# Performance work log

Measured on AMD Instinct MI355X. Metric: run time of the kernel, lower is better.

Reference implementation:

```python
import jax, jax.numpy as jnp
import numpy as np

N_NODES = 100000
N_EDGES = 3200000
VM, VA, PG, QG, PD, QD = 0, 1, 2, 3, 4, 5
G, B = 0, 1


def setup_inputs() -> dict:
    key = jax.random.key(0)
    k1, k2, k3, k4, k5 = jax.random.split(key, 5)
    pred = jax.random.normal(k1, (N_NODES, 6), dtype=jnp.float32)
    target = jax.random.normal(k2, (N_NODES, 6), dtype=jnp.float32)
    edge_index = jax.random.randint(k3, (2, N_EDGES), 0, N_NODES, dtype=jnp.int64)
    edge_attr = jax.random.normal(k4, (N_EDGES, 2), dtype=jnp.float32)
    mask = jax.random.randint(k5, (N_NODES, 6), 0, 2) == 1
    return {"pred": pred, "target": target, "edge_index": edge_index,
            "edge_attr": edge_attr, "mask": mask}


def reference(pred, target, edge_index, edge_attr, mask):
    # temp_pred[~mask] = target[~mask]
    temp_pred = jnp.where(mask, pred, target)
    vm = temp_pred[:, VM]
    va = temp_pred[:, VA]
    pg = temp_pred[:, PG]
    qg = temp_pred[:, QG]
    pd = temp_pred[:, PD]
    qd = temp_pred[:, QD]
    g = edge_attr[:, G]
    b = edge_attr[:, B]
    src, dst = edge_index[0], edge_index[1]

    v_from = vm[src]                      # [E] gather
    v_to = vm[dst]
    ang = va[src] - va[dst]
    c, s = jnp.cos(ang), jnp.sin(ang)
    vv = v_from * v_to
    p_flow = vv * (g * c + b * s)         # [E]
    q_flow = vv * (g * s - b * c)

    # scatter-add flows into source nodes
    p_calc = jax.ops.segment_sum(p_flow, src, num_segments=N_NODES)
    q_calc = jax.ops.segment_sum(q_flow, src, num_segments=N_NODES)

    p_imb = pg - pd - p_calc
    q_imb = qg - qd - q_calc
    loss = jnp.mean(p_imb ** 2) + jnp.mean(q_imb ** 2)
    return loss
```

## Files before the change

kernel.cpp:

```cpp
#include <hip/hip_runtime.h>
#include <cstdint>

#define N_NODES 100000
#define N_EDGES 3200000
#define SPAN    256
#define SHIFT   8
#define NB      ((N_NODES + SPAN - 1) / SPAN)
#define CHUNK   4096
#define BTH     512
#define NITER   (CHUNK / BTH)
#define NBLK    ((N_EDGES + CHUNK - 1) / CHUNK)
#define PREF_W  (NB + 1)

__global__ __launch_bounds__(256)
void prep_kernel(const float* __restrict__ pred,
                 const float* __restrict__ target,
                 const void* __restrict__ mask,
                 float2* __restrict__ u_tab,
                 float2* __restrict__ base_pq,
                 float* __restrict__ d_out, int out_size) {
    __shared__ int s_mask8;
    if (threadIdx.x < 64) {
        uint32_t w = ((const uint32_t*)mask)[threadIdx.x];
        bool nz = (w & 0xFFFFFF00u) != 0u;
        unsigned long long m = __ballot(nz);
        if (threadIdx.x == 0) s_mask8 = (m != 0ull) ? 1 : 0;
    }
    if (blockIdx.x == 0 && threadIdx.x == 0)
        for (int k = 0; k < out_size; ++k) d_out[k] = 0.0f;
    __syncthreads();

    int i = blockIdx.x * 256 + threadIdx.x;
    if (i >= N_NODES) return;

    const float2* p2 = (const float2*)pred;
    const float2* t2 = (const float2*)target;
    float2 pa = p2[3 * i], pb = p2[3 * i + 1], pc = p2[3 * i + 2];
    float2 ta = t2[3 * i], tb = t2[3 * i + 1], tc = t2[3 * i + 2];
    float pr[6] = {pa.x, pa.y, pb.x, pb.y, pc.x, pc.y};
    float tg[6] = {ta.x, ta.y, tb.x, tb.y, tc.x, tc.y};
    int mk[6];
    if (s_mask8) {
        const uint16_t* mu = (const uint16_t*)mask;
        uint16_t m0 = mu[3 * i], m1 = mu[3 * i + 1], m2 = mu[3 * i + 2];
        mk[0] = m0 & 0xFF; mk[1] = m0 >> 8;
        mk[2] = m1 & 0xFF; mk[3] = m1 >> 8;
        mk[4] = m2 & 0xFF; mk[5] = m2 >> 8;
    } else {
        const int2* mi = (const int2*)mask;
        int2 m0 = mi[3 * i], m1 = mi[3 * i + 1], m2 = mi[3 * i + 2];
        mk[0] = m0.x; mk[1] = m0.y; mk[2] = m1.x;
        mk[3] = m1.y; mk[4] = m2.x; mk[5] = m2.y;
    }
    float tp[6];
    #pragma unroll
    for (int j = 0; j < 6; ++j) tp[j] = mk[j] ? pr[j] : tg[j];

    float s, c;
    sincosf(tp[1], &s, &c);
    u_tab[i]   = make_float2(tp[0] * c, tp[0] * s);
    base_pq[i] = make_float2(tp[2] - tp[4], tp[3] - tp[5]);
}

__global__ __launch_bounds__(BTH)
void bin_kernel(const void* __restrict__ edge_index,
                const float2* __restrict__ edge_attr,
                const float2* __restrict__ u_tab,
                uint2* __restrict__ recs,
                uint16_t* __restrict__ pref_T) {
    __shared__ uint2 s_rec[CHUNK];
    __shared__ uint32_t s_cnt[NB];
    __shared__ uint32_t s_pref[PREF_W];
    __shared__ uint32_t s_wsum[8], s_woff[8];
    __shared__ int s_i64;

    const int tid = threadIdx.x;
    const int lane = tid & 63, wid = tid >> 6;
    if (tid < 64) {
        uint32_t w = ((const uint32_t*)edge_index)[tid];
        bool nz = (tid & 1) && (w != 0u);
        unsigned long long m = __ballot(nz);
        if (tid == 0) s_i64 = (m == 0ull) ? 1 : 0;
    }
    if (tid < NB) s_cnt[tid] = 0u;
    __syncthreads();
    const bool is64 = (s_i64 != 0);
    const int ebase = blockIdx.x * CHUNK;
    const int nE = min(CHUNK, N_EDGES - ebase);

    uint32_t src_r[NITER];
    #pragma unroll
    for (int it = 0; it < NITER; ++it) {
        int j = it * BTH + tid;
        uint32_t s = 0u;
        if (j < nE) {
            int e = ebase + j;
            s = is64 ? (uint32_t)((const unsigned long long*)edge_index)[e]
                     : ((const uint32_t*)edge_index)[e];
            atomicAdd(&s_cnt[s >> SHIFT], 1u);
        }
        src_r[it] = s;
    }
    __syncthreads();

    {
        uint32_t v0 = (tid < NB) ? s_cnt[tid] : 0u;
        uint32_t x = v0;
        #pragma unroll
        for (int off = 1; off < 64; off <<= 1) {
            uint32_t y = (uint32_t)__shfl_up((int)x, off, 64);
            if (lane >= off) x += y;
        }
        if (lane == 63) s_wsum[wid] = x;
        __syncthreads();
        if (tid < 8) {
            uint32_t w0 = s_wsum[tid];
            uint32_t xx = w0;
            #pragma unroll
            for (int off = 1; off < 8; off <<= 1) {
                uint32_t y = (uint32_t)__shfl_up((int)xx, off, 64);
                if (tid >= off) xx += y;
            }
            s_woff[tid] = xx - w0;
        }
        __syncthreads();
        uint32_t incl = x + s_woff[wid];
        if (tid < NB) s_pref[tid + 1] = incl;
        if (tid == 0) s_pref[0] = 0u;
        if (tid < NB) s_cnt[tid] = 0u;
        __syncthreads();
    }

    #pragma unroll
    for (int it = 0; it < NITER; ++it) {
        int j = it * BTH + tid;
        if (j < nE) {
            int e = ebase + j;
            uint32_t dst = is64
                ? (uint32_t)((const unsigned long long*)edge_index)[(size_t)N_EDGES + e]
                : ((const uint32_t*)edge_index)[(size_t)N_EDGES + e];
            float2 gb = edge_attr[e];
            float2 u  = u_tab[dst];
            float vr = gb.x * u.x - gb.y * u.y;
            float vi = -(gb.y * u.x + gb.x * u.y);
            uint32_t nid = src_r[it];
            uint32_t bk = nid >> SHIFT, lid = nid & (SPAN - 1);
            uint32_t r = atomicAdd(&s_cnt[bk], 1u);
            uint2 rc;
            rc.x = (__float_as_uint(vr) & ~0xFFu) | lid;
            rc.y = __float_as_uint(vi);
            s_rec[s_pref[bk] + r] = rc;
        }
    }
    __syncthreads();

    {
        const uint4* s4 = (const uint4*)s_rec;
        uint4* a4 = (uint4*)(recs + (size_t)blockIdx.x * CHUNK);
        for (int k = tid; k < nE / 2; k += BTH) a4[k] = s4[k];
        if ((nE & 1) && tid == 0)
            recs[(size_t)blockIdx.x * CHUNK + nE - 1] = s_rec[nE - 1];
    }
    for (int b = tid; b < PREF_W; b += BTH)
        pref_T[(size_t)b * NBLK + blockIdx.x] = (uint16_t)s_pref[b];
}

__global__ __launch_bounds__(1024)
void reduce_kernel(const uint2* __restrict__ recs,
                   const uint16_t* __restrict__ pref_T,
                   const float2* __restrict__ u_tab,
                   const float2* __restrict__ base_pq,
                   float* __restrict__ d_out) {
    __shared__ float2 s_acc[4][SPAN];
    __shared__ float s_part[16];
    if (threadIdx.x < SPAN) {
        #pragma unroll
        for (int r = 0; r < 4; ++r) s_acc[r][threadIdx.x] = make_float2(0.0f, 0.0f);
    }
    __syncthreads();

    const int b = blockIdx.x;
    const int rep = (threadIdx.x >> 6) & 3;
    if (threadIdx.x < NBLK) {
        uint32_t s = pref_T[(size_t)b * NBLK + threadIdx.x];
        uint32_t e = pref_T[(size_t)(b + 1) * NBLK + threadIdx.x];
        const uint2* arena = recs + (size_t)threadIdx.x * CHUNK;
        uint32_t j = s;
        for (; j + 2 <= e; j += 2) {
            uint2 r0 = arena[j];
            uint2 r1 = arena[j + 1];
            atomicAdd(&s_acc[rep][r0.x & 0xFFu].x, __uint_as_float(r0.x & ~0xFFu));
            atomicAdd(&s_acc[rep][r0.x & 0xFFu].y, __uint_as_float(r0.y));
            atomicAdd(&s_acc[rep][r1.x & 0xFFu].x, __uint_as_float(r1.x & ~0xFFu));
            atomicAdd(&s_acc[rep][r1.x & 0xFFu].y, __uint_as_float(r1.y));
        }
        if (j < e) {
            uint2 rc = arena[j];
            atomicAdd(&s_acc[rep][rc.x & 0xFFu].x, __uint_as_float(rc.x & ~0xFFu));
            atomicAdd(&s_acc[rep][rc.x & 0xFFu].y, __uint_as_float(rc.y));
        }
    }
    __syncthreads();

    float v = 0.0f;
    int node = b * SPAN + (int)threadIdx.x;
    if (threadIdx.x < SPAN && node < N_NODES) {
        float2 S = make_float2(0.0f, 0.0f);
        #pragma unroll
        for (int rr = 0; rr < 4; ++rr) {
            float2 t = s_acc[rr][threadIdx.x];
            S.x += t.x; S.y += t.y;
        }
        float2 ui = u_tab[node];
        float2 bp = base_pq[node];
        float pc = ui.x * S.x - ui.y * S.y;
        float qc = ui.x * S.y + ui.y * S.x;
        float p = bp.x - pc, q = bp.y - qc;
        v = p * p + q * q;
    }
    #pragma unroll
    for (int off = 32; off > 0; off >>= 1) v += __shfl_down(v, off, 64);
    if ((threadIdx.x & 63) == 0) s_part[threadIdx.x >> 6] = v;
    __syncthreads();
    if (threadIdx.x == 0) {
        float t = 0.0f;
        #pragma unroll
        for (int w = 0; w < 16; ++w) t += s_part[w];
        atomicAdd(d_out, t * (1.0f / (float)N_NODES));
    }
}

extern "C" void kernel_launch(void* const* d_in, const int* in_sizes, int n_in,
                              void* d_out, int out_size, void* d_ws, size_t ws_size,
                              hipStream_t stream) {
    const float*  pred       = (const float*)d_in[0];
    const float*  target     = (const float*)d_in[1];
    const void*   edge_index = d_in[2];
    const float2* edge_attr  = (const float2*)d_in[3];
    const void*   mask       = d_in[4];
    float* out = (float*)d_out;

    char* ws = (char*)d_ws;
    float2*   u_tab   = (float2*)ws;
    float2*   base_pq = (float2*)(ws + 800000);
    uint16_t* pref_T  = (uint16_t*)(ws + 1600000);
    uint2*    recs    = (uint2*)(ws + 2400000);

    prep_kernel<<<(N_NODES + 255) / 256, 256, 0, stream>>>(
        pred, target, mask, u_tab, base_pq, out, out_size);

    bin_kernel<<<NBLK, BTH, 0, stream>>>(
        edge_index, edge_attr, u_tab, recs, pref_T);

    reduce_kernel<<<NB, 1024, 0, stream>>>(
        recs, pref_T, u_tab, base_pq, out);
}
```

Measured before the change: 173.9 us.

## Double bin chunk size and split each reduce segment across two threads

The binning chunk grows to 8192 edges with 1024-thread blocks. This halves the number of producer blocks and the size of the transposed prefix table, and lets the record arena move closer in the workspace. In the reduce kernel, each producer segment is split between two threads, so 782 threads stay busy despite fewer producers. Each thread reads records pairwise with 16-byte loads after aligning to an even index. The risks are lower bin-kernel block count (391 blocks), heavier LDS use per block, and dropping the odd-tail store, which relies on every chunk length being even.

```diff
diff --git a/kernel.cpp b/kernel.cpp
--- a/kernel.cpp
+++ b/kernel.cpp
@@ -6,8 +6,8 @@
 #define SPAN    256
 #define SHIFT   8
 #define NB      ((N_NODES + SPAN - 1) / SPAN)
-#define CHUNK   4096
-#define BTH     512
+#define CHUNK   8192
+#define BTH     1024
 #define NITER   (CHUNK / BTH)
 #define NBLK    ((N_EDGES + CHUNK - 1) / CHUNK)
 #define PREF_W  (NB + 1)
@@ -71,7 +71,7 @@
     __shared__ uint2 s_rec[CHUNK];
     __shared__ uint32_t s_cnt[NB];
     __shared__ uint32_t s_pref[PREF_W];
-    __shared__ uint32_t s_wsum[8], s_woff[8];
+    __shared__ uint32_t s_wsum[16], s_woff[16];
     __shared__ int s_i64;
 
     const int tid = threadIdx.x;
@@ -113,11 +113,11 @@
         }
         if (lane == 63) s_wsum[wid] = x;
         __syncthreads();
-        if (tid < 8) {
+        if (tid < 16) {
             uint32_t w0 = s_wsum[tid];
             uint32_t xx = w0;
             #pragma unroll
-            for (int off = 1; off < 8; off <<= 1) {
+            for (int off = 1; off < 16; off <<= 1) {
                 uint32_t y = (uint32_t)__shfl_up((int)xx, off, 64);
                 if (tid >= off) xx += y;
             }
@@ -158,8 +158,6 @@
         const uint4* s4 = (const uint4*)s_rec;
         uint4* a4 = (uint4*)(recs + (size_t)blockIdx.x * CHUNK);
         for (int k = tid; k < nE / 2; k += BTH) a4[k] = s4[k];
-        if ((nE & 1) && tid == 0)
-            recs[(size_t)blockIdx.x * CHUNK + nE - 1] = s_rec[nE - 1];
     }
     for (int b = tid; b < PREF_W; b += BTH)
         pref_T[(size_t)b * NBLK + blockIdx.x] = (uint16_t)s_pref[b];
@@ -181,18 +179,26 @@
 
     const int b = blockIdx.x;
     const int rep = (threadIdx.x >> 6) & 3;
-    if (threadIdx.x < NBLK) {
-        uint32_t s = pref_T[(size_t)b * NBLK + threadIdx.x];
-        uint32_t e = pref_T[(size_t)(b + 1) * NBLK + threadIdx.x];
-        const uint2* arena = recs + (size_t)threadIdx.x * CHUNK;
-        uint32_t j = s;
+    if (threadIdx.x < 2 * NBLK) {
+        const int prod = (threadIdx.x < NBLK) ? threadIdx.x : threadIdx.x - NBLK;
+        const int half = (threadIdx.x < NBLK) ? 0 : 1;
+        uint32_t s0 = pref_T[(size_t)b * NBLK + prod];
+        uint32_t e0 = pref_T[(size_t)(b + 1) * NBLK + prod];
+        uint32_t mid = s0 + ((e0 - s0 + 1) >> 1);
+        uint32_t j = half ? mid : s0;
+        uint32_t e = half ? e0 : mid;
+        const uint2* arena = recs + (size_t)prod * CHUNK;
+        if (j < e && (j & 1)) {
+            uint2 rc = arena[j++];
+            atomicAdd(&s_acc[rep][rc.x & 0xFFu].x, __uint_as_float(rc.x & ~0xFFu));
+            atomicAdd(&s_acc[rep][rc.x & 0xFFu].y, __uint_as_float(rc.y));
+        }
         for (; j + 2 <= e; j += 2) {
-            uint2 r0 = arena[j];
-            uint2 r1 = arena[j + 1];
-            atomicAdd(&s_acc[rep][r0.x & 0xFFu].x, __uint_as_float(r0.x & ~0xFFu));
-            atomicAdd(&s_acc[rep][r0.x & 0xFFu].y, __uint_as_float(r0.y));
-            atomicAdd(&s_acc[rep][r1.x & 0xFFu].x, __uint_as_float(r1.x & ~0xFFu));
-            atomicAdd(&s_acc[rep][r1.x & 0xFFu].y, __uint_as_float(r1.y));
+            uint4 q = *(const uint4*)&arena[j];
+            atomicAdd(&s_acc[rep][q.x & 0xFFu].x, __uint_as_float(q.x & ~0xFFu));
+            atomicAdd(&s_acc[rep][q.x & 0xFFu].y, __uint_as_float(q.y));
+            atomicAdd(&s_acc[rep][q.z & 0xFFu].x, __uint_as_float(q.z & ~0xFFu));
+            atomicAdd(&s_acc[rep][q.z & 0xFFu].y, __uint_as_float(q.w));
         }
         if (j < e) {
             uint2 rc = arena[j];
@@ -244,7 +250,7 @@
     float2*   u_tab   = (float2*)ws;
     float2*   base_pq = (float2*)(ws + 800000);
     uint16_t* pref_T  = (uint16_t*)(ws + 1600000);
-    uint2*    recs    = (uint2*)(ws + 2400000);
+    uint2*    recs    = (uint2*)(ws + 1906560);
 
     prep_kernel<<<(N_NODES + 255) / 256, 256, 0, stream>>>(
         pred, target, mask, u_tab, base_pq, out, out_size);
```

Result: slower. 177.7 us (+2.2%).
